# Kernel optimization log

Hardware: AMD Instinct MI355X
Metric: run time of the kernel (lower is better)

The kernel has to match this reference:

```python
import jax, jax.numpy as jnp
import numpy as np

NUM_GRAPHS = 256
BN_EPS = 1e-5


def setup_inputs() -> dict:
    key = jax.random.key(0)
    ks = jax.random.split(key, 16)
    N, E, D_IN, D, L = 100000, 1200000, 4, 64, 3
    inp = {
        "x": jax.random.normal(ks[0], (N, D_IN), dtype=jnp.float32),
        "EdgeID": jax.random.randint(ks[1], (2, E), 0, N, dtype=jnp.int64),
        "EdgeAttr": jax.random.uniform(ks[2], (E,), dtype=jnp.float32),
        "batch": jnp.sort(jax.random.randint(ks[3], (N,), 0, NUM_GRAPHS, dtype=jnp.int64)),
        # embedding Linear(4, 64)
        "W_emb": jax.random.normal(ks[4], (D_IN, D), dtype=jnp.float32) * 0.5,
        "b_emb": jax.random.normal(ks[5], (D,), dtype=jnp.float32) * 0.1,
        # LEConv params stacked over layers: lin1 (bias), lin2 (no bias), lin3 (bias)
        "W1": jax.random.normal(ks[6], (L, D, D), dtype=jnp.float32) * 0.125,
        "b1": jax.random.normal(ks[7], (L, D), dtype=jnp.float32) * 0.1,
        "W2": jax.random.normal(ks[8], (L, D, D), dtype=jnp.float32) * 0.125,
        "W3": jax.random.normal(ks[9], (L, D, D), dtype=jnp.float32) * 0.125,
        "b3": jax.random.normal(ks[10], (L, D), dtype=jnp.float32) * 0.1,
        # BatchNorm affine params per layer
        "gamma": jnp.ones((L, D), dtype=jnp.float32),
        "beta": jnp.zeros((L, D), dtype=jnp.float32),
        # MLP head
        "W_l1": jax.random.normal(ks[11], (D, D), dtype=jnp.float32) * 0.125,
        "b_l1": jax.random.normal(ks[12], (D,), dtype=jnp.float32) * 0.1,
        "W_l2": jax.random.normal(ks[13], (D, 3), dtype=jnp.float32) * 0.125,
        "b_l2": jax.random.normal(ks[14], (3,), dtype=jnp.float32) * 0.1,
    }
    return inp


def reference(x, EdgeID, EdgeAttr, batch, W_emb, b_emb, W1, b1, W2, W3, b3,
              gamma, beta, W_l1, b_l1, W_l2, b_l2):
    N = x.shape[0]
    L = W1.shape[0]
    src, dst = EdgeID[0], EdgeID[1]  # message flows src(j) -> dst(i)

    h = x @ W_emb + b_emb  # [N, 64]; F.dropout(training=False) is a no-op
    for i in range(L):
        a = h @ W1[i] + b1[i]               # lin1(x_j)
        b = h @ W2[i]                       # lin2(x_i)
        msg = EdgeAttr[:, None] * (a[src] - b[dst])  # [E, 64]
        agg = jax.ops.segment_sum(msg, dst, num_segments=N)
        h = agg + h @ W3[i] + b3[i]         # LEConv output
        # BatchNorm (training-mode batch stats over nodes)
        mean = jnp.mean(h, axis=0)
        var = jnp.var(h, axis=0)
        h = gamma[i] * (h - mean) * jax.lax.rsqrt(var + BN_EPS) + beta[i]
        h = jax.nn.relu(h)

    # global mean pool over graphs
    ones = jnp.ones((N,), dtype=h.dtype)
    counts = jax.ops.segment_sum(ones, batch, num_segments=NUM_GRAPHS)
    sums = jax.ops.segment_sum(h, batch, num_segments=NUM_GRAPHS)
    g = sums / jnp.maximum(counts, 1.0)[:, None]  # [G, 64]

    pred = jax.nn.relu(g @ W_l1 + b_l1) @ W_l2 + b_l2  # [G, 3]
    return pred
```

## Files before the change

kernel.cpp:

```cpp
#include <hip/hip_runtime.h>

#define BN_EPS 1e-5f

typedef __attribute__((ext_vector_type(8))) short bf16x8;
typedef __attribute__((ext_vector_type(4))) float f32x4;

__global__ void k_hist(const int* __restrict__ dst, int* __restrict__ deg, int E) {
    int e = blockIdx.x * blockDim.x + threadIdx.x;
    if (e < E) atomicAdd(&deg[dst[e]], 1);
}

__global__ __launch_bounds__(256) void k_blocksum(const int* __restrict__ deg,
                                                  int* __restrict__ bsum, int N) {
    __shared__ int red[256];
    int tid = threadIdx.x;
    int base = blockIdx.x * 1024 + tid * 4;
    int s = 0;
    if (base + 3 < N) {
        int4 v = *(const int4*)&deg[base];
        s = v.x + v.y + v.z + v.w;
    } else {
        for (int i = 0; i < 4; ++i) if (base + i < N) s += deg[base + i];
    }
    red[tid] = s;
    __syncthreads();
    for (int d = 128; d > 0; d >>= 1) {
        if (tid < d) red[tid] += red[tid + d];
        __syncthreads();
    }
    if (tid == 0) bsum[blockIdx.x] = red[0];
}

__global__ __launch_bounds__(1024) void k_scanpartials(int* __restrict__ bsum, int nb) {
    __shared__ int t[1024];
    int tid = threadIdx.x;
    int v = (tid < nb) ? bsum[tid] : 0;
    t[tid] = v;
    __syncthreads();
    for (int d = 1; d < 1024; d <<= 1) {
        int u = (tid >= d) ? t[tid - d] : 0;
        __syncthreads();
        t[tid] += u;
        __syncthreads();
    }
    if (tid < nb) bsum[tid] = t[tid] - v;
}

__global__ __launch_bounds__(256) void k_applyscan(const int* __restrict__ deg,
                                                   const int* __restrict__ bsum,
                                                   int* __restrict__ rowptr,
                                                   int* __restrict__ gcur, int N, int E) {
    __shared__ int red[256];
    int tid = threadIdx.x;
    int base = blockIdx.x * 1024 + tid * 4;
    int v0 = 0, v1 = 0, v2 = 0, v3 = 0;
    if (base + 3 < N) {
        int4 v = *(const int4*)&deg[base];
        v0 = v.x; v1 = v.y; v2 = v.z; v3 = v.w;
    } else {
        if (base < N) v0 = deg[base];
        if (base + 1 < N) v1 = deg[base + 1];
        if (base + 2 < N) v2 = deg[base + 2];
        if (base + 3 < N) v3 = deg[base + 3];
    }
    int s = v0 + v1 + v2 + v3;
    red[tid] = s;
    __syncthreads();
    for (int d = 1; d < 256; d <<= 1) {
        int u = (tid >= d) ? red[tid - d] : 0;
        __syncthreads();
        red[tid] += u;
        __syncthreads();
    }
    int off = bsum[blockIdx.x] + red[tid] - s;
    int r0 = off, r1 = off + v0, r2 = r1 + v1, r3 = r2 + v2;
    if (base < N)     rowptr[base] = r0;
    if (base + 1 < N) rowptr[base + 1] = r1;
    if (base + 2 < N) rowptr[base + 2] = r2;
    if (base + 3 < N) rowptr[base + 3] = r3;
    if ((base & 255) == 0 && base < N) gcur[base >> 8] = r0;
    if (blockIdx.x == 0 && tid == 0) rowptr[N] = E;
}

#define ABLK 8192
__global__ __launch_bounds__(1024) void k_binA(const int* __restrict__ src,
                                               const int* __restrict__ dst,
                                               const float* __restrict__ attr,
                                               int* __restrict__ gcur,
                                               unsigned long long* __restrict__ tmp,
                                               int E, int N) {
    __shared__ int hist[1024];
    __shared__ int lcur[1024];
    int tid = threadIdx.x;
    int NB = (N + 255) >> 8;
    int e0 = blockIdx.x * ABLK;
    int e1 = e0 + ABLK; if (e1 > E) e1 = E;
    for (int i = tid; i < NB; i += 1024) hist[i] = 0;
    __syncthreads();
    for (int e = e0 + tid; e < e1; e += 1024) atomicAdd(&hist[dst[e] >> 8], 1);
    __syncthreads();
    for (int b = tid; b < NB; b += 1024) {
        int hc = hist[b];
        lcur[b] = hc ? atomicAdd(&gcur[b], hc) : 0;
    }
    __syncthreads();
    for (int e = e0 + tid; e < e1; e += 1024) {
        int d = dst[e];
        int pos = atomicAdd(&lcur[d >> 8], 1);
        unsigned long long p = ((unsigned long long)__float_as_uint(attr[e]) << 32) |
                               ((unsigned long long)(d & 255) << 24) |
                               (unsigned int)src[e];
        tmp[pos] = p;
    }
}

__global__ __launch_bounds__(256) void k_binB(const int* __restrict__ rowptr,
                                              const unsigned long long* __restrict__ tmp,
                                              unsigned long long* __restrict__ edata,
                                              int N) {
    __shared__ int cur[256];
    int b = blockIdx.x;
    int tid = threadIdx.x;
    int nb0 = b << 8;
    int node = nb0 + tid;
    cur[tid] = (node < N) ? rowptr[node] : 0;
    int beg = rowptr[nb0];
    int endnode = nb0 + 256; if (endnode > N) endnode = N;
    int end = rowptr[endnode];
    __syncthreads();
    for (int e = beg + tid; e < end; e += 256) {
        unsigned long long p = tmp[e];
        int dl = (int)((p >> 24) & 255);
        int pos = atomicAdd(&cur[dl], 1);
        edata[pos] = (p & 0xFFFFFFFF00000000ull) | (p & 0xFFFFFFull);
    }
}

__device__ __forceinline__ void bn_coeff(const float* bs, const float* gam,
                                         const float* bet, int c, float inv_n,
                                         float& sc, float& sh) {
    float mean = bs[c] * inv_n;
    float var = bs[64 + c] * inv_n - mean * mean;
    sc = gam[c] * rsqrtf(fmaxf(var, 0.f) + BN_EPS);
    sh = bet[c] - mean * sc;
}

__device__ __forceinline__ float h16lo(unsigned u) {
    return (float)__builtin_bit_cast(_Float16, (unsigned short)(u & 0xFFFFu));
}
__device__ __forceinline__ float h16hi(unsigned u) {
    return (float)__builtin_bit_cast(_Float16, (unsigned short)(u >> 16));
}

__global__ void k_gather4(const int* __restrict__ rowptr,
                          const unsigned long long* __restrict__ edata,
                          const float* __restrict__ x,
                          float* __restrict__ g4, float* __restrict__ degw, int N) {
    int n = blockIdx.x * blockDim.x + threadIdx.x;
    if (n >= N) return;
    int beg = rowptr[n], end = rowptr[n + 1];
    float4 a0 = {0.f, 0.f, 0.f, 0.f}, a1 = {0.f, 0.f, 0.f, 0.f};
    float wsum = 0.f;
    int e = beg;
    for (; e + 1 < end; e += 2) {
        unsigned long long p0 = edata[e], p1 = edata[e + 1];
        float w0 = __uint_as_float((unsigned)(p0 >> 32));
        float w1 = __uint_as_float((unsigned)(p1 >> 32));
        float4 v0 = *(const float4*)((const char*)x + (((unsigned)p0) << 4));
        float4 v1 = *(const float4*)((const char*)x + (((unsigned)p1) << 4));
        a0.x += w0 * v0.x; a0.y += w0 * v0.y; a0.z += w0 * v0.z; a0.w += w0 * v0.w;
        a1.x += w1 * v1.x; a1.y += w1 * v1.y; a1.z += w1 * v1.z; a1.w += w1 * v1.w;
        wsum += w0 + w1;
    }
    if (e < end) {
        unsigned long long p0 = edata[e];
        float w0 = __uint_as_float((unsigned)(p0 >> 32));
        float4 v0 = *(const float4*)((const char*)x + (((unsigned)p0) << 4));
        a0.x += w0 * v0.x; a0.y += w0 * v0.y; a0.z += w0 * v0.z; a0.w += w0 * v0.w;
        wsum += w0;
    }
    float4 r;
    r.x = a0.x + a1.x; r.y = a0.y + a1.y; r.z = a0.z + a1.z; r.w = a0.w + a1.w;
    *(float4*)&g4[(size_t)n * 4] = r;
    degw[n] = wsum;
}

__global__ __launch_bounds__(256) void k_act(const float* __restrict__ h,
                                             const float* __restrict__ bs,
                                             const float* __restrict__ gam,
                                             const float* __restrict__ bet,
                                             unsigned short* __restrict__ a16,
                                             int N) {
    __shared__ float scS[64], shS[64];
    int tid = threadIdx.x;
    if (tid < 64) {
        float sc, sh;
        bn_coeff(bs, gam, bet, tid, 1.f / (float)N, sc, sh);
        scS[tid] = sc; shS[tid] = sh;
    }
    __syncthreads();
    int c0 = (tid & 15) << 2;
    float4 scv = *(const float4*)&scS[c0];
    float4 shv = *(const float4*)&shS[c0];
    int total = N << 4;
    for (int t = blockIdx.x * 256 + tid; t < total; t += gridDim.x * 256) {
        float4 v = *(const float4*)&h[(size_t)t * 4];
        float r0 = fmaxf(fmaf(v.x, scv.x, shv.x), 0.f);
        float r1 = fmaxf(fmaf(v.y, scv.y, shv.y), 0.f);
        float r2 = fmaxf(fmaf(v.z, scv.z, shv.z), 0.f);
        float r3 = fmaxf(fmaf(v.w, scv.w, shv.w), 0.f);
        unsigned q0 = __builtin_bit_cast(unsigned short, (_Float16)r0);
        unsigned q1 = __builtin_bit_cast(unsigned short, (_Float16)r1);
        unsigned q2 = __builtin_bit_cast(unsigned short, (_Float16)r2);
        unsigned q3 = __builtin_bit_cast(unsigned short, (_Float16)r3);
        uint2 o; o.x = q0 | (q1 << 16); o.y = q2 | (q3 << 16);
        *(uint2*)&a16[(size_t)t * 4] = o;
    }
}

__global__ void k_gather16(const int* __restrict__ rowptr,
                           const unsigned long long* __restrict__ edata,
                           const unsigned short* __restrict__ a16,
                           float* __restrict__ S, int N) {
    int t = blockIdx.x * blockDim.x + threadIdx.x;
    int n = t >> 6, c = t & 63;
    if (n >= N) return;
    unsigned c2 = (unsigned)(c << 1);
    int beg = rowptr[n], end = rowptr[n + 1];
    int len = end - beg;
    float acc[8] = {0.f, 0.f, 0.f, 0.f, 0.f, 0.f, 0.f, 0.f};
    int nFull = len & ~7;
    for (int base = 0; base < nFull; base += 8) {
#pragma unroll
        for (int i = 0; i < 8; ++i) {
            unsigned long long p = edata[beg + base + i];
            float w = __uint_as_float((unsigned)(p >> 32));
            unsigned off = ((unsigned)p) << 7;
            float v = (float)*(const _Float16*)((const char*)a16 + (off | c2));
            acc[i] = fmaf(w, v, acc[i]);
        }
    }
    if (nFull < len) {
#pragma unroll
        for (int i = 0; i < 8; ++i) {
            int idx = nFull + i;
            unsigned long long p = edata[beg + (idx < len ? idx : len - 1)];
            float w = (idx < len) ? __uint_as_float((unsigned)(p >> 32)) : 0.f;
            unsigned off = ((unsigned)p) << 7;
            float v = (float)*(const _Float16*)((const char*)a16 + (off | c2));
            acc[i] = fmaf(w, v, acc[i]);
        }
    }
    float r = ((acc[0] + acc[1]) + (acc[2] + acc[3])) +
              ((acc[4] + acc[5]) + (acc[6] + acc[7]));
    S[(size_t)n * 64 + c] = r;
}

__device__ __forceinline__ void split_pack8(const float* v, uint4& H, uint4& L) {
    unsigned hb[8], lb[8];
#pragma unroll
    for (int j = 0; j < 8; ++j) {
        unsigned b = __float_as_uint(v[j]);
        unsigned rb = (b + 0x7FFFu + ((b >> 16) & 1u)) & 0xFFFF0000u;
        hb[j] = rb >> 16;
        float lo = v[j] - __uint_as_float(rb);
        lb[j] = __float_as_uint(lo) >> 16;
    }
    H.x = hb[0] | (hb[1] << 16); H.y = hb[2] | (hb[3] << 16);
    H.z = hb[4] | (hb[5] << 16); H.w = hb[6] | (hb[7] << 16);
    L.x = lb[0] | (lb[1] << 16); L.y = lb[2] | (lb[3] << 16);
    L.z = lb[4] | (lb[5] << 16); L.w = lb[6] | (lb[7] << 16);
}

__device__ __forceinline__ void split_frag(const float* w, bf16x8& hi, bf16x8& lo) {
#pragma unroll
    for (int j = 0; j < 8; ++j) {
        unsigned b = __float_as_uint(w[j]);
        unsigned rb = (b + 0x7FFFu + ((b >> 16) & 1u)) & 0xFFFF0000u;
        hi[j] = (short)(rb >> 16);
        float lof = w[j] - __uint_as_float(rb);
        lo[j] = (short)(__float_as_uint(lof) >> 16);
    }
}

template <int PRE, int EMB>
__global__ __launch_bounds__(512) void k_update(
    const float* __restrict__ S, float* __restrict__ h,
    const float* __restrict__ degw,
    const float* __restrict__ xin, const float* __restrict__ g4,
    const float* __restrict__ Wemb, const float* __restrict__ bemb,
    const unsigned short* __restrict__ a16,
    const float* __restrict__ W1, const float* __restrict__ b1,
    const float* __restrict__ W2, const float* __restrict__ W3,
    const float* __restrict__ b3,
    float* __restrict__ bnstats, int N) {
    __shared__ __align__(16) unsigned short sA[16384];
    __shared__ float dwS[64];

    int tid = threadIdx.x;
    int lane = tid & 63;
    int wv = tid >> 6;
    int mg = wv >> 2;
    int nb = wv & 3;
    int c = (nb << 4) | (lane & 15);
    int krow = (lane >> 4) << 3;

    bf16x8 B1h[2], B1l[2], B2h[2], B2l[2], B3h[2], B3l[2];
#pragma unroll
    for (int ks = 0; ks < 2; ++ks) {
        float w1v[8], w2v[8], w3v[8];
        int kb = ks * 32 + krow;
#pragma unroll
        for (int j = 0; j < 8; ++j) {
            int idx = (kb + j) * 64 + c;
            w1v[j] = W1[idx];
            w2v[j] = W2[idx];
            w3v[j] = W3[idx];
        }
        split_frag(w1v, B1h[ks], B1l[ks]);
        split_frag(w2v, B2h[ks], B2l[ks]);
        split_frag(w3v, B3h[ks], B3l[ks]);
    }
    float b1c = b1[c], b3c = b3[c];

    int r = tid >> 3;
    int kg = tid & 7;
    int k0 = kg << 3;
    int slot = ((((r >> 4) * 2 + (kg >> 2)) * 64) + ((kg & 3) << 4) + (r & 15)) * 8;

    float we0[8], we1[8], we2[8], we3[8], bev[8];
    if (EMB) {
#pragma unroll
        for (int j = 0; j < 8; ++j) {
            we0[j] = Wemb[k0 + j];
            we1[j] = Wemb[64 + k0 + j];
            we2[j] = Wemb[128 + k0 + j];
            we3[j] = Wemb[192 + k0 + j];
            bev[j] = bemb[k0 + j];
        }
    }

    float bsum = 0.f, bsq = 0.f;
    int numTiles = (N + 63) >> 6;
    for (int tile = blockIdx.x; tile < numTiles; tile += gridDim.x) {
        int n0 = tile << 6;
        __syncthreads();
        {
            int n = n0 + r;
            float sv[8], hv[8];
            if (n < N) {
                if (EMB) {
                    float4 g = *(const float4*)&g4[(size_t)n * 4];
                    float4 xr = *(const float4*)&xin[(size_t)n * 4];
                    float dw = degw[n];
#pragma unroll
                    for (int j = 0; j < 8; ++j) {
                        sv[j] = fmaf(g.x, we0[j], fmaf(g.y, we1[j],
                                 fmaf(g.z, we2[j], fmaf(g.w, we3[j], dw * bev[j]))));
                        hv[j] = fmaf(xr.x, we0[j], fmaf(xr.y, we1[j],
                                 fmaf(xr.z, we2[j], fmaf(xr.w, we3[j], bev[j]))));
                    }
                } else {
                    const float* Sp = &S[(size_t)n * 64 + k0];
                    float4 s0_ = *(const float4*)Sp;
                    float4 s1_ = *(const float4*)(Sp + 4);
                    sv[0]=s0_.x; sv[1]=s0_.y; sv[2]=s0_.z; sv[3]=s0_.w;
                    sv[4]=s1_.x; sv[5]=s1_.y; sv[6]=s1_.z; sv[7]=s1_.w;
                    uint4 hp = *(const uint4*)((const char*)a16 + (((size_t)n) << 7) + (k0 << 1));
                    hv[0] = h16lo(hp.x); hv[1] = h16hi(hp.x);
                    hv[2] = h16lo(hp.y); hv[3] = h16hi(hp.y);
                    hv[4] = h16lo(hp.z); hv[5] = h16hi(hp.z);
                    hv[6] = h16lo(hp.w); hv[7] = h16hi(hp.w);
                }
            } else {
#pragma unroll
                for (int j = 0; j < 8; ++j) { sv[j] = 0.f; hv[j] = 0.f; }
            }
            uint4 H, L;
            split_pack8(sv, H, L);
            *(uint4*)&sA[slot] = H;
            *(uint4*)&sA[4096 + slot] = L;
            split_pack8(hv, H, L);
            *(uint4*)&sA[8192 + slot] = H;
            *(uint4*)&sA[12288 + slot] = L;
            if (tid < 64) dwS[tid] = (n0 + tid < N) ? degw[n0 + tid] : 0.f;
        }
        __syncthreads();
        f32x4 accP[2] = {{0.f,0.f,0.f,0.f},{0.f,0.f,0.f,0.f}};
        f32x4 accN[2] = {{0.f,0.f,0.f,0.f},{0.f,0.f,0.f,0.f}};
#pragma unroll
        for (int ks = 0; ks < 2; ++ks) {
#pragma unroll
            for (int mtg = 0; mtg < 2; ++mtg) {
                int mt = mg * 2 + mtg;
                int base = ((mt * 2 + ks) * 64 + lane) * 8;
                bf16x8 aSh = *(const bf16x8*)&sA[base];
                bf16x8 aSl = *(const bf16x8*)&sA[4096 + base];
                bf16x8 aHh = *(const bf16x8*)&sA[8192 + base];
                bf16x8 aHl = *(const bf16x8*)&sA[12288 + base];
                f32x4 p = accP[mtg], q = accN[mtg];
                p = __builtin_amdgcn_mfma_f32_16x16x32_bf16(aSh, B1h[ks], p, 0, 0, 0);
                p = __builtin_amdgcn_mfma_f32_16x16x32_bf16(aSl, B1h[ks], p, 0, 0, 0);
                p = __builtin_amdgcn_mfma_f32_16x16x32_bf16(aSh, B1l[ks], p, 0, 0, 0);
                p = __builtin_amdgcn_mfma_f32_16x16x32_bf16(aHh, B3h[ks], p, 0, 0, 0);
                p = __builtin_amdgcn_mfma_f32_16x16x32_bf16(aHl, B3h[ks], p, 0, 0, 0);
                p = __builtin_amdgcn_mfma_f32_16x16x32_bf16(aHh, B3l[ks], p, 0, 0, 0);
                q = __builtin_amdgcn_mfma_f32_16x16x32_bf16(aHh, B2h[ks], q, 0, 0, 0);
                q = __builtin_amdgcn_mfma_f32_16x16x32_bf16(aHl, B2h[ks], q, 0, 0, 0);
                q = __builtin_amdgcn_mfma_f32_16x16x32_bf16(aHh, B2l[ks], q, 0, 0, 0);
                accP[mtg] = p; accN[mtg] = q;
            }
        }
#pragma unroll
        for (int mtg = 0; mtg < 2; ++mtg) {
            int rowb = mg * 32 + mtg * 16 + ((lane >> 4) << 2);
            float4 dwv = *(const float4*)&dwS[rowb];
            float dwa[4] = {dwv.x, dwv.y, dwv.z, dwv.w};
#pragma unroll
            for (int j = 0; j < 4; ++j) {
                int n = n0 + rowb + j;
                if (n < N) {
                    float val = accP[mtg][j] - dwa[j] * accN[mtg][j] + dwa[j] * b1c + b3c;
                    h[(size_t)n * 64 + c] = val;
                    bsum += val;
                    bsq += val * val;
                }
            }
        }
    }
    __syncthreads();
    float* red = (float*)sA;
    red[tid] = bsum;
    red[512 + tid] = bsq;
    __syncthreads();
    if (tid < 64) {
        int nb_ = tid >> 4, cl = tid & 15;
        float s = 0.f, qq = 0.f;
#pragma unroll
        for (int i = 0; i < 8; ++i) {
            int t = ((i & 1) << 8) + (nb_ << 6) + ((i >> 1) << 4) + cl;
            s += red[t];
            qq += red[512 + t];
        }
        atomicAdd(&bnstats[tid], s);
        atomicAdd(&bnstats[64 + tid], qq);
    }
}

#define POOL_TILE 128
__global__ __launch_bounds__(256) void k_poolsum(const float* __restrict__ h,
                                                 const int* __restrict__ batch,
                                                 const float* __restrict__ bsp,
                                                 const float* __restrict__ gamp,
                                                 const float* __restrict__ betp,
                                                 float* __restrict__ gsums, int N) {
    int tid = threadIdx.x;
    int c = tid & 63, q = tid >> 6;
    float sc, sh_;
    bn_coeff(bsp, gamp, betp, c, 1.f / (float)N, sc, sh_);
    int n0 = blockIdx.x * POOL_TILE;
    int nEnd = n0 + POOL_TILE; if (nEnd > N) nEnd = N;
    int g = -1;
    float acc = 0.f;
    for (int n = n0 + q; n < nEnd; n += 4) {
        int b = batch[n];
        if (b != g) {
            if (g >= 0) atomicAdd(&gsums[(size_t)g * 64 + c], acc);
            g = b; acc = 0.f;
        }
        acc += fmaxf(fmaf(h[(size_t)n * 64 + c], sc, sh_), 0.f);
    }
    if (g >= 0) atomicAdd(&gsums[(size_t)g * 64 + c], acc);
}

__global__ void k_head(const float* __restrict__ gsums, const int* __restrict__ batch,
                       const float* __restrict__ Wl1, const float* __restrict__ bl1,
                       const float* __restrict__ Wl2, const float* __restrict__ bl2,
                       float* __restrict__ out, int N) {
    int g = blockIdx.x;
    int c = threadIdx.x;
    int lo = 0, hi = N;
    while (lo < hi) { int mid = (lo + hi) >> 1; if (batch[mid] < g) lo = mid + 1; else hi = mid; }
    int start = lo;
    hi = N;
    while (lo < hi) { int mid = (lo + hi) >> 1; if (batch[mid] < g + 1) lo = mid + 1; else hi = mid; }
    int cnt = lo - start;
    float denom = (float)(cnt > 0 ? cnt : 1);
    __shared__ float gS[64], yS[64];
    gS[c] = gsums[(size_t)g * 64 + c] / denom;
    __syncthreads();
    float y = bl1[c];
    for (int k = 0; k < 64; ++k) y += gS[k] * Wl1[k * 64 + c];
    yS[c] = fmaxf(y, 0.f);
    __syncthreads();
    if (c < 3) {
        float o = bl2[c];
        for (int k = 0; k < 64; ++k) o += yS[k] * Wl2[k * 3 + c];
        out[g * 3 + c] = o;
    }
}

extern "C" void kernel_launch(void* const* d_in, const int* in_sizes, int n_in,
                              void* d_out, int out_size, void* d_ws, size_t ws_size,
                              hipStream_t stream) {
    const float* x     = (const float*)d_in[0];
    const int*   eid   = (const int*)d_in[1];
    const float* attr  = (const float*)d_in[2];
    const int*   batch = (const int*)d_in[3];
    const float* Wemb  = (const float*)d_in[4];
    const float* bemb  = (const float*)d_in[5];
    const float* W1    = (const float*)d_in[6];
    const float* b1    = (const float*)d_in[7];
    const float* W2    = (const float*)d_in[8];
    const float* W3    = (const float*)d_in[9];
    const float* b3    = (const float*)d_in[10];
    const float* gamma = (const float*)d_in[11];
    const float* beta  = (const float*)d_in[12];
    const float* Wl1   = (const float*)d_in[13];
    const float* bl1   = (const float*)d_in[14];
    const float* Wl2   = (const float*)d_in[15];
    const float* bl2   = (const float*)d_in[16];

    int N = in_sizes[3];
    int E = in_sizes[2];
    int L = in_sizes[7] / 64;
    int G = out_size / 3;

    const int* src = eid;
    const int* dst = eid + E;

    float* ws      = (float*)d_ws;
    float* h       = ws;
    float* S       = h + (size_t)N * 64;
    float* degw    = S + (size_t)N * 64;
    float* g4      = degw + N;
    float* bnstats = g4 + (size_t)N * 4;
    float* gsums   = bnstats + 3 * 128;
    int*   deg     = (int*)(gsums + (size_t)G * 64);
    int*   rowptr  = deg + N;
    int*   bsum    = rowptr + (N + 2);
    int*   gcur    = bsum + 1024;
    unsigned long long* edata = (unsigned long long*)(gcur + 1024);
    unsigned long long* tmp   = edata + E;
    unsigned short* a16 = (unsigned short*)(((uintptr_t)(tmp + E) + 15) & ~(uintptr_t)15);

    int nScanBlocks = (N + 1023) / 1024;
    int NB = (N + 255) >> 8;

    hipMemsetAsync(deg, 0, (size_t)N * sizeof(int), stream);
    hipMemsetAsync(bnstats, 0, 3 * 128 * sizeof(float), stream);
    k_hist<<<(E + 255) / 256, 256, 0, stream>>>(dst, deg, E);
    k_blocksum<<<nScanBlocks, 256, 0, stream>>>(deg, bsum, N);
    k_scanpartials<<<1, 1024, 0, stream>>>(bsum, nScanBlocks);
    k_applyscan<<<nScanBlocks, 256, 0, stream>>>(deg, bsum, rowptr, gcur, N, E);
    k_binA<<<(E + ABLK - 1) / ABLK, 1024, 0, stream>>>(src, dst, attr, gcur, tmp, E, N);
    k_binB<<<NB, 256, 0, stream>>>(rowptr, tmp, edata, N);

    int gGrid = (N * 64 + 255) / 256;
    for (int l = 0; l < L; ++l) {
        if (l == 0) {
            k_gather4<<<(N + 255) / 256, 256, 0, stream>>>(rowptr, edata, x, g4, degw, N);
            k_update<0, 1><<<512, 512, 0, stream>>>(S, h, degw, x, g4, Wemb, bemb,
                                                    nullptr,
                                                    W1, b1, W2, W3, b3, bnstats, N);
        } else {
            k_gather16<<<gGrid, 256, 0, stream>>>(rowptr, edata, a16, S, N);
            k_update<1, 0><<<512, 512, 0, stream>>>(S, h, degw, nullptr, nullptr,
                                                    nullptr, nullptr, a16,
                                                    W1 + (size_t)l * 4096, b1 + (size_t)l * 64,
                                                    W2 + (size_t)l * 4096, W3 + (size_t)l * 4096,
                                                    b3 + (size_t)l * 64,
                                                    bnstats + (size_t)l * 128, N);
        }
        if (l + 1 < L) {
            k_act<<<1024, 256, 0, stream>>>(h, bnstats + (size_t)l * 128,
                                            gamma + (size_t)l * 64, beta + (size_t)l * 64,
                                            a16, N);
        }
    }

    hipMemsetAsync(gsums, 0, (size_t)G * 64 * sizeof(float), stream);
    k_poolsum<<<(N + POOL_TILE - 1) / POOL_TILE, 256, 0, stream>>>(
        h, batch, bnstats + (size_t)(L - 1) * 128, gamma + (size_t)(L - 1) * 64,
        beta + (size_t)(L - 1) * 64, gsums, N);
    k_head<<<G, 64, 0, stream>>>(gsums, batch, Wl1, bl1, Wl2, bl2, (float*)d_out, N);
}
```

Measured before the change: 427.8 us.

## Split fp16 activations into four channel planes and gather per plane pass

The activation buffer is stored as four planes of 16 channels each instead of row-major 64 channels, and the gather kernel makes four passes, one per plane. Each wave handles one node, with 8 edge groups times 8 channel pairs, and the partial sums are combined by shuffle reduction. The aim is to make each pass's gathered working set (N×32 bytes) small enough to stay in cache and to replace 2-byte loads with 4-byte loads. The cost is that edge data is read four times, plus the added shuffle reduction and the use of nontemporal loads and stores.

Result: slower. 595.8 us (+39.3%).

```diff
diff --git a/kernel.cpp b/kernel.cpp
--- a/kernel.cpp
+++ b/kernel.cpp
@@ -204,6 +204,7 @@
     float4 shv = *(const float4*)&shS[c0];
     int total = N << 4;
     for (int t = blockIdx.x * 256 + tid; t < total; t += gridDim.x * 256) {
+        int n = t >> 4, qc = t & 15;
         float4 v = *(const float4*)&h[(size_t)t * 4];
         float r0 = fmaxf(fmaf(v.x, scv.x, shv.x), 0.f);
         float r1 = fmaxf(fmaf(v.y, scv.y, shv.y), 0.f);
@@ -214,46 +215,42 @@
         unsigned q2 = __builtin_bit_cast(unsigned short, (_Float16)r2);
         unsigned q3 = __builtin_bit_cast(unsigned short, (_Float16)r3);
         uint2 o; o.x = q0 | (q1 << 16); o.y = q2 | (q3 << 16);
-        *(uint2*)&a16[(size_t)t * 4] = o;
-    }
-}
-
-__global__ void k_gather16(const int* __restrict__ rowptr,
-                           const unsigned long long* __restrict__ edata,
-                           const unsigned short* __restrict__ a16,
-                           float* __restrict__ S, int N) {
-    int t = blockIdx.x * blockDim.x + threadIdx.x;
-    int n = t >> 6, c = t & 63;
+        size_t dst = (size_t)(qc >> 2) * ((size_t)N * 16) + (size_t)n * 16 + ((qc & 3) << 2);
+        *(uint2*)&a16[dst] = o;
+    }
+}
+
+__global__ __launch_bounds__(256) void k_gatherP(const int* __restrict__ rowptr,
+                                                 const unsigned long long* __restrict__ edata,
+                                                 const unsigned short* __restrict__ a16,
+                                                 float* __restrict__ S, int N,
+                                                 int blocksPerPass) {
+    int pass = blockIdx.x / blocksPerPass;
+    int n = (blockIdx.x - pass * blocksPerPass) * 4 + (threadIdx.x >> 6);
     if (n >= N) return;
-    unsigned c2 = (unsigned)(c << 1);
+    int lane = threadIdx.x & 63;
+    int j = lane >> 3;
+    int cp = lane & 7;
+    const char* plane = (const char*)(a16 + (size_t)pass * ((size_t)N * 16));
+    unsigned c4 = (unsigned)(cp << 2);
     int beg = rowptr[n], end = rowptr[n + 1];
-    int len = end - beg;
-    float acc[8] = {0.f, 0.f, 0.f, 0.f, 0.f, 0.f, 0.f, 0.f};
-    int nFull = len & ~7;
-    for (int base = 0; base < nFull; base += 8) {
-#pragma unroll
-        for (int i = 0; i < 8; ++i) {
-            unsigned long long p = edata[beg + base + i];
-            float w = __uint_as_float((unsigned)(p >> 32));
-            unsigned off = ((unsigned)p) << 7;
-            float v = (float)*(const _Float16*)((const char*)a16 + (off | c2));
-            acc[i] = fmaf(w, v, acc[i]);
-        }
-    }
-    if (nFull < len) {
-#pragma unroll
-        for (int i = 0; i < 8; ++i) {
-            int idx = nFull + i;
-            unsigned long long p = edata[beg + (idx < len ? idx : len - 1)];
-            float w = (idx < len) ? __uint_as_float((unsigned)(p >> 32)) : 0.f;
-            unsigned off = ((unsigned)p) << 7;
-            float v = (float)*(const _Float16*)((const char*)a16 + (off | c2));
-            acc[i] = fmaf(w, v, acc[i]);
-        }
-    }
-    float r = ((acc[0] + acc[1]) + (acc[2] + acc[3])) +
-              ((acc[4] + acc[5]) + (acc[6] + acc[7]));
-    S[(size_t)n * 64 + c] = r;
+    float a0 = 0.f, a1 = 0.f;
+    for (int e = beg + j; e < end; e += 8) {
+        unsigned long long p = __builtin_nontemporal_load(&edata[e]);
+        float w = __uint_as_float((unsigned)(p >> 32));
+        unsigned off = (((unsigned)p) << 5) | c4;
+        unsigned v = *(const unsigned*)(plane + off);
+        a0 = fmaf(w, h16lo(v), a0);
+        a1 = fmaf(w, h16hi(v), a1);
+    }
+    a0 += __shfl_xor(a0, 8);  a1 += __shfl_xor(a1, 8);
+    a0 += __shfl_xor(a0, 16); a1 += __shfl_xor(a1, 16);
+    a0 += __shfl_xor(a0, 32); a1 += __shfl_xor(a1, 32);
+    if (j == 0) {
+        float* dst = &S[(size_t)n * 64 + (pass << 4) + (cp << 1)];
+        __builtin_nontemporal_store(a0, dst);
+        __builtin_nontemporal_store(a1, dst + 1);
+    }
 }
 
 __device__ __forceinline__ void split_pack8(const float* v, uint4& H, uint4& L) {
@@ -339,6 +336,12 @@
             bev[j] = bemb[k0 + j];
         }
     }
+    const unsigned short* aPlane = nullptr;
+    int aOff = 0;
+    if (PRE) {
+        aPlane = a16 + (size_t)(kg >> 1) * ((size_t)N * 16);
+        aOff = (kg & 1) << 3;
+    }
 
     float bsum = 0.f, bsq = 0.f;
     int numTiles = (N + 63) >> 6;
@@ -366,7 +369,7 @@
                     float4 s1_ = *(const float4*)(Sp + 4);
                     sv[0]=s0_.x; sv[1]=s0_.y; sv[2]=s0_.z; sv[3]=s0_.w;
                     sv[4]=s1_.x; sv[5]=s1_.y; sv[6]=s1_.z; sv[7]=s1_.w;
-                    uint4 hp = *(const uint4*)((const char*)a16 + (((size_t)n) << 7) + (k0 << 1));
+                    uint4 hp = *(const uint4*)&aPlane[(size_t)n * 16 + aOff];
                     hv[0] = h16lo(hp.x); hv[1] = h16hi(hp.x);
                     hv[2] = h16lo(hp.y); hv[3] = h16hi(hp.y);
                     hv[4] = h16lo(hp.z); hv[5] = h16hi(hp.z);
@@ -556,7 +559,7 @@
     k_binA<<<(E + ABLK - 1) / ABLK, 1024, 0, stream>>>(src, dst, attr, gcur, tmp, E, N);
     k_binB<<<NB, 256, 0, stream>>>(rowptr, tmp, edata, N);
 
-    int gGrid = (N * 64 + 255) / 256;
+    int blocksPerPass = (N + 3) / 4;
     for (int l = 0; l < L; ++l) {
         if (l == 0) {
             k_gather4<<<(N + 255) / 256, 256, 0, stream>>>(rowptr, edata, x, g4, degw, N);
@@ -564,7 +567,8 @@
                                                     nullptr,
                                                     W1, b1, W2, W3, b3, bnstats, N);
         } else {
-            k_gather16<<<gGrid, 256, 0, stream>>>(rowptr, edata, a16, S, N);
+            k_gatherP<<<blocksPerPass * 4, 256, 0, stream>>>(rowptr, edata, a16, S, N,
+                                                             blocksPerPass);
             k_update<1, 0><<<512, 512, 0, stream>>>(S, h, degw, nullptr, nullptr,
                                                     nullptr, nullptr, a16,
                                                     W1 + (size_t)l * 4096, b1 + (size_t)l * 64,
```

## Sort edges by source within 128-node dst buckets and aggregate in LDS

Applied to the files above, without the earlier changes.

Edge binning now uses 128-node destination buckets. Within each bucket, edges are sorted by a coarse source key (src>>8) instead of by exact destination, which is meant to improve locality of the gathered source rows. The gather kernels now process a whole bucket per block and accumulate per-destination sums in shared memory with atomics, replacing the per-node CSR walk. This trades per-node sequential reduction for LDS float atomics and bucket-level load balance. It also makes the floating-point summation order nondeterministic.

Measured after the change: 1.375 ms. 3.21x slower.

```diff
diff --git a/kernel.cpp b/kernel.cpp
--- a/kernel.cpp
+++ b/kernel.cpp
@@ -78,7 +78,7 @@
     if (base + 1 < N) rowptr[base + 1] = r1;
     if (base + 2 < N) rowptr[base + 2] = r2;
     if (base + 3 < N) rowptr[base + 3] = r3;
-    if ((base & 255) == 0 && base < N) gcur[base >> 8] = r0;
+    if ((base & 127) == 0 && base < N) gcur[base >> 7] = r0;
     if (blockIdx.x == 0 && tid == 0) rowptr[N] = E;
 }
 
@@ -92,12 +92,12 @@
     __shared__ int hist[1024];
     __shared__ int lcur[1024];
     int tid = threadIdx.x;
-    int NB = (N + 255) >> 8;
+    int NB = (N + 127) >> 7;
     int e0 = blockIdx.x * ABLK;
     int e1 = e0 + ABLK; if (e1 > E) e1 = E;
     for (int i = tid; i < NB; i += 1024) hist[i] = 0;
     __syncthreads();
-    for (int e = e0 + tid; e < e1; e += 1024) atomicAdd(&hist[dst[e] >> 8], 1);
+    for (int e = e0 + tid; e < e1; e += 1024) atomicAdd(&hist[dst[e] >> 7], 1);
     __syncthreads();
     for (int b = tid; b < NB; b += 1024) {
         int hc = hist[b];
@@ -106,33 +106,48 @@
     __syncthreads();
     for (int e = e0 + tid; e < e1; e += 1024) {
         int d = dst[e];
-        int pos = atomicAdd(&lcur[d >> 8], 1);
+        int pos = atomicAdd(&lcur[d >> 7], 1);
         unsigned long long p = ((unsigned long long)__float_as_uint(attr[e]) << 32) |
-                               ((unsigned long long)(d & 255) << 24) |
+                               ((unsigned long long)(d & 127) << 24) |
                                (unsigned int)src[e];
         tmp[pos] = p;
     }
 }
 
-__global__ __launch_bounds__(256) void k_binB(const int* __restrict__ rowptr,
-                                              const unsigned long long* __restrict__ tmp,
-                                              unsigned long long* __restrict__ edata,
-                                              int N) {
-    __shared__ int cur[256];
+__global__ __launch_bounds__(512) void k_binB2(const int* __restrict__ rowptr,
+                                               const unsigned long long* __restrict__ tmp,
+                                               unsigned long long* __restrict__ edata,
+                                               int N) {
+    __shared__ int hist[512];
+    __shared__ int scn[512];
+    __shared__ int cur[512];
     int b = blockIdx.x;
     int tid = threadIdx.x;
-    int nb0 = b << 8;
-    int node = nb0 + tid;
-    cur[tid] = (node < N) ? rowptr[node] : 0;
+    int nb0 = b << 7;
     int beg = rowptr[nb0];
-    int endnode = nb0 + 256; if (endnode > N) endnode = N;
+    int endnode = nb0 + 128; if (endnode > N) endnode = N;
     int end = rowptr[endnode];
-    __syncthreads();
-    for (int e = beg + tid; e < end; e += 256) {
+    hist[tid] = 0;
+    __syncthreads();
+    for (int e = beg + tid; e < end; e += 512)
+        atomicAdd(&hist[((unsigned)tmp[e] & 0xFFFFFFu) >> 8], 1);
+    __syncthreads();
+    int v = hist[tid];
+    scn[tid] = v;
+    __syncthreads();
+    for (int d = 1; d < 512; d <<= 1) {
+        int u = (tid >= d) ? scn[tid - d] : 0;
+        __syncthreads();
+        scn[tid] += u;
+        __syncthreads();
+    }
+    cur[tid] = beg + scn[tid] - v;
+    __syncthreads();
+    for (int e = beg + tid; e < end; e += 512) {
         unsigned long long p = tmp[e];
-        int dl = (int)((p >> 24) & 255);
-        int pos = atomicAdd(&cur[dl], 1);
-        edata[pos] = (p & 0xFFFFFFFF00000000ull) | (p & 0xFFFFFFull);
+        int sb = ((unsigned)p & 0xFFFFFFu) >> 8;
+        int pos = atomicAdd(&cur[sb], 1);
+        edata[pos] = p;
     }
 }
 
@@ -152,37 +167,47 @@
     return (float)__builtin_bit_cast(_Float16, (unsigned short)(u >> 16));
 }
 
-__global__ void k_gather4(const int* __restrict__ rowptr,
-                          const unsigned long long* __restrict__ edata,
-                          const float* __restrict__ x,
-                          float* __restrict__ g4, float* __restrict__ degw, int N) {
-    int n = blockIdx.x * blockDim.x + threadIdx.x;
-    if (n >= N) return;
-    int beg = rowptr[n], end = rowptr[n + 1];
-    float4 a0 = {0.f, 0.f, 0.f, 0.f}, a1 = {0.f, 0.f, 0.f, 0.f};
-    float wsum = 0.f;
-    int e = beg;
-    for (; e + 1 < end; e += 2) {
-        unsigned long long p0 = edata[e], p1 = edata[e + 1];
-        float w0 = __uint_as_float((unsigned)(p0 >> 32));
-        float w1 = __uint_as_float((unsigned)(p1 >> 32));
-        float4 v0 = *(const float4*)((const char*)x + (((unsigned)p0) << 4));
-        float4 v1 = *(const float4*)((const char*)x + (((unsigned)p1) << 4));
-        a0.x += w0 * v0.x; a0.y += w0 * v0.y; a0.z += w0 * v0.z; a0.w += w0 * v0.w;
-        a1.x += w1 * v1.x; a1.y += w1 * v1.y; a1.z += w1 * v1.z; a1.w += w1 * v1.w;
-        wsum += w0 + w1;
-    }
-    if (e < end) {
-        unsigned long long p0 = edata[e];
-        float w0 = __uint_as_float((unsigned)(p0 >> 32));
-        float4 v0 = *(const float4*)((const char*)x + (((unsigned)p0) << 4));
-        a0.x += w0 * v0.x; a0.y += w0 * v0.y; a0.z += w0 * v0.z; a0.w += w0 * v0.w;
-        wsum += w0;
-    }
-    float4 r;
-    r.x = a0.x + a1.x; r.y = a0.y + a1.y; r.z = a0.z + a1.z; r.w = a0.w + a1.w;
-    *(float4*)&g4[(size_t)n * 4] = r;
-    degw[n] = wsum;
+__global__ __launch_bounds__(256) void k_gather4S(const int* __restrict__ rowptr,
+                                                  const unsigned long long* __restrict__ edata,
+                                                  const float* __restrict__ x,
+                                                  float* __restrict__ g4,
+                                                  float* __restrict__ degw, int N) {
+    __shared__ float acc4[512];
+    __shared__ float dwacc[128];
+    int b = blockIdx.x;
+    int tid = threadIdx.x;
+    int nb0 = b << 7;
+    int beg = rowptr[nb0];
+    int endnode = nb0 + 128; if (endnode > N) endnode = N;
+    int end = rowptr[endnode];
+    for (int i = tid; i < 512; i += 256) acc4[i] = 0.f;
+    if (tid < 128) dwacc[tid] = 0.f;
+    __syncthreads();
+    int lane = tid & 63;
+    int w = tid >> 6;
+    int el = lane >> 2;
+    int ch = lane & 3;
+    for (int base = beg + w * 32; base < end; base += 128) {
+#pragma unroll
+        for (int j = 0; j < 2; ++j) {
+            int e = base + j * 16 + el;
+            unsigned long long p = (e < end) ? edata[e] : 0ull;
+            float wt = __uint_as_float((unsigned)(p >> 32));
+            unsigned srcb = ((unsigned)p & 0xFFFFFFu);
+            float v = *(const float*)((const char*)x + (srcb << 4) + (ch << 2));
+            int dl = (int)((p >> 24) & 127u);
+            atomicAdd(&acc4[dl * 4 + ch], wt * v);
+            if (ch == 0) atomicAdd(&dwacc[dl], wt);
+        }
+    }
+    __syncthreads();
+    if (tid < 128) {
+        int n = nb0 + tid;
+        if (n < N) {
+            *(float4*)&g4[(size_t)n * 4] = *(float4*)&acc4[tid * 4];
+            degw[n] = dwacc[tid];
+        }
+    }
 }
 
 __global__ __launch_bounds__(256) void k_act(const float* __restrict__ h,
@@ -218,42 +243,47 @@
     }
 }
 
-__global__ void k_gather16(const int* __restrict__ rowptr,
-                           const unsigned long long* __restrict__ edata,
-                           const unsigned short* __restrict__ a16,
-                           float* __restrict__ S, int N) {
-    int t = blockIdx.x * blockDim.x + threadIdx.x;
-    int n = t >> 6, c = t & 63;
-    if (n >= N) return;
-    unsigned c2 = (unsigned)(c << 1);
-    int beg = rowptr[n], end = rowptr[n + 1];
-    int len = end - beg;
-    float acc[8] = {0.f, 0.f, 0.f, 0.f, 0.f, 0.f, 0.f, 0.f};
-    int nFull = len & ~7;
-    for (int base = 0; base < nFull; base += 8) {
-#pragma unroll
-        for (int i = 0; i < 8; ++i) {
-            unsigned long long p = edata[beg + base + i];
-            float w = __uint_as_float((unsigned)(p >> 32));
-            unsigned off = ((unsigned)p) << 7;
-            float v = (float)*(const _Float16*)((const char*)a16 + (off | c2));
-            acc[i] = fmaf(w, v, acc[i]);
-        }
-    }
-    if (nFull < len) {
-#pragma unroll
-        for (int i = 0; i < 8; ++i) {
-            int idx = nFull + i;
-            unsigned long long p = edata[beg + (idx < len ? idx : len - 1)];
-            float w = (idx < len) ? __uint_as_float((unsigned)(p >> 32)) : 0.f;
-            unsigned off = ((unsigned)p) << 7;
-            float v = (float)*(const _Float16*)((const char*)a16 + (off | c2));
-            acc[i] = fmaf(w, v, acc[i]);
-        }
-    }
-    float r = ((acc[0] + acc[1]) + (acc[2] + acc[3])) +
-              ((acc[4] + acc[5]) + (acc[6] + acc[7]));
-    S[(size_t)n * 64 + c] = r;
+__global__ __launch_bounds__(512) void k_gatherS(const int* __restrict__ rowptr,
+                                                 const unsigned long long* __restrict__ edata,
+                                                 const unsigned short* __restrict__ a16,
+                                                 float* __restrict__ S, int N) {
+    __shared__ float acc[8192];
+    int b = blockIdx.x;
+    int tid = threadIdx.x;
+    int nb0 = b << 7;
+    int beg = rowptr[nb0];
+    int endnode = nb0 + 128; if (endnode > N) endnode = N;
+    int end = rowptr[endnode];
+    {
+        float4 z = {0.f, 0.f, 0.f, 0.f};
+        for (int i = tid; i < 2048; i += 512) *(float4*)&acc[i * 4] = z;
+    }
+    __syncthreads();
+    int lane = tid & 63;
+    int u = ((tid >> 6) << 1) | ((lane >> 5) & 1);
+    int cp = lane & 31;
+    for (int base = beg + u * 4; base < end; base += 64) {
+        unsigned long long p0 = edata[base];
+        unsigned long long p1 = (base + 1 < end) ? edata[base + 1] : 0ull;
+        unsigned long long p2 = (base + 2 < end) ? edata[base + 2] : 0ull;
+        unsigned long long p3 = (base + 3 < end) ? edata[base + 3] : 0ull;
+#pragma unroll
+        for (int j = 0; j < 4; ++j) {
+            unsigned long long p = (j == 0) ? p0 : (j == 1) ? p1 : (j == 2) ? p2 : p3;
+            float wt = __uint_as_float((unsigned)(p >> 32));
+            unsigned off = (((unsigned)p & 0xFFFFFFu) << 7) | (cp << 2);
+            unsigned v = *(const unsigned*)((const char*)a16 + off);
+            int dl = (int)((p >> 24) & 127u);
+            atomicAdd(&acc[dl * 64 + (cp << 1)], wt * h16lo(v));
+            atomicAdd(&acc[dl * 64 + (cp << 1) + 1], wt * h16hi(v));
+        }
+    }
+    __syncthreads();
+    for (int i = tid; i < 2048; i += 512) {
+        int idx = i * 4;
+        int n = nb0 + (idx >> 6);
+        if (n < N) *(float4*)&S[(size_t)n * 64 + (idx & 63)] = *(float4*)&acc[idx];
+    }
 }
 
 __device__ __forceinline__ void split_pack8(const float* v, uint4& H, uint4& L) {
@@ -545,7 +575,7 @@
     unsigned short* a16 = (unsigned short*)(((uintptr_t)(tmp + E) + 15) & ~(uintptr_t)15);
 
     int nScanBlocks = (N + 1023) / 1024;
-    int NB = (N + 255) >> 8;
+    int NB = (N + 127) >> 7;
 
     hipMemsetAsync(deg, 0, (size_t)N * sizeof(int), stream);
     hipMemsetAsync(bnstats, 0, 3 * 128 * sizeof(float), stream);
@@ -554,17 +584,16 @@
     k_scanpartials<<<1, 1024, 0, stream>>>(bsum, nScanBlocks);
     k_applyscan<<<nScanBlocks, 256, 0, stream>>>(deg, bsum, rowptr, gcur, N, E);
     k_binA<<<(E + ABLK - 1) / ABLK, 1024, 0, stream>>>(src, dst, attr, gcur, tmp, E, N);
-    k_binB<<<NB, 256, 0, stream>>>(rowptr, tmp, edata, N);
-
-    int gGrid = (N * 64 + 255) / 256;
+    k_binB2<<<NB, 512, 0, stream>>>(rowptr, tmp, edata, N);
+
     for (int l = 0; l < L; ++l) {
         if (l == 0) {
-            k_gather4<<<(N + 255) / 256, 256, 0, stream>>>(rowptr, edata, x, g4, degw, N);
+            k_gather4S<<<NB, 256, 0, stream>>>(rowptr, edata, x, g4, degw, N);
             k_update<0, 1><<<512, 512, 0, stream>>>(S, h, degw, x, g4, Wemb, bemb,
                                                     nullptr,
                                                     W1, b1, W2, W3, b3, bnstats, N);
         } else {
-            k_gather16<<<gGrid, 256, 0, stream>>>(rowptr, edata, a16, S, N);
+            k_gatherS<<<NB, 512, 0, stream>>>(rowptr, edata, a16, S, N);
             k_update<1, 0><<<512, 512, 0, stream>>>(S, h, degw, nullptr, nullptr,
                                                     nullptr, nullptr, a16,
                                                     W1 + (size_t)l * 4096, b1 + (size_t)l * 64,
```
